# Optimization experiments

Hardware: AMD Instinct MI355X
Metric: run time of the kernel (lower is better)

## Reference

```python
import jax, jax.numpy as jnp
import numpy as np

B, S, D = 4, 2048, 1024
E, F = 8, 4096


def setup_inputs() -> dict:
    key = jax.random.key(0)
    ks = jax.random.split(key, 5)
    x = jax.random.normal(ks[0], (B, S, D), dtype=jnp.float32)
    switch_w = jax.random.normal(ks[1], (D, E), dtype=jnp.float32) * (D ** -0.5)
    switch_b = jnp.zeros((E,), dtype=jnp.float32)
    w1 = jax.random.normal(ks[2], (E, D, F), dtype=jnp.float32) * (D ** -0.5)
    b1 = jnp.zeros((E, F), dtype=jnp.float32)
    w2 = jax.random.normal(ks[3], (E, F, D), dtype=jnp.float32) * (F ** -0.5)
    b2 = jnp.zeros((E, D), dtype=jnp.float32)
    return {"x": x, "switch_w": switch_w, "switch_b": switch_b,
            "w1": w1, "b1": b1, "w2": w2, "b2": b2}


def reference(x, switch_w, switch_b, w1, b1, w2, b2):
    b, s, d = x.shape
    t = x.reshape(-1, d)                                  # [T, D] tokens
    logits = t @ switch_w + switch_b                      # [T, E]
    route_prob = jax.nn.softmax(logits, axis=-1)
    route_prob_max = jnp.max(route_prob, axis=-1)         # [T]
    routes = jnp.argmax(route_prob, axis=-1)              # [T] top-1 expert

    out = jnp.zeros_like(t)
    n_experts = w1.shape[0]
    for e in range(n_experts):                            # small fixed expert loop
        h = jax.nn.gelu(t @ w1[e] + b1[e])                # [T, F]
        y = h @ w2[e] + b2[e]                             # [T, D]
        mask = (routes == e)[:, None]
        out = jnp.where(mask, y, out)                     # scatter-combine by route

    out = out * route_prob_max[:, None]                   # is_scale_prob=True
    return out.reshape(b, s, d)
```

## Files before the change

kernel.cpp:

```cpp
#include <hip/hip_runtime.h>
#include <hip/hip_bf16.h>
#include <math.h>

#define T_TOK 8192
#define DIM   1024
#define NEXP  8
#define FF    4096
#define BM    256
#define BN    256
#define BK    64
#define TPAD  (T_TOK + NEXP * BM)
#define NCBLK 32
#define MT    (TPAD / BM)
#define NG1   640
#define NG2   160
#define NT2   4096

typedef __attribute__((ext_vector_type(4))) float  f32x4;
typedef __attribute__((ext_vector_type(8))) __bf16 bf16x8;
typedef __attribute__((address_space(3))) char ldschar;

__global__ __launch_bounds__(256) void router_kernel(const float* __restrict__ x,
                              const float* __restrict__ sw, const float* __restrict__ sb,
                              int* __restrict__ route, float* __restrict__ scale,
                              __hip_bfloat16* __restrict__ xb)
{
    int wave = threadIdx.x >> 6, lane = threadIdx.x & 63;
    int t = blockIdx.x * 4 + wave;
    const float* xr = x + (size_t)t * DIM + lane * 16;

    float xv[16];
#pragma unroll
    for (int i = 0; i < 4; ++i)
        *(float4*)&xv[i * 4] = *(const float4*)(xr + i * 4);

    bf16x8 u0, u1;
#pragma unroll
    for (int i = 0; i < 8; ++i) { u0[i] = (__bf16)xv[i]; u1[i] = (__bf16)xv[i + 8]; }
    __hip_bfloat16* xo = xb + (size_t)t * DIM + lane * 16;
    *(bf16x8*)xo = u0;
    *(bf16x8*)(xo + 8) = u1;

    double acc[NEXP];
#pragma unroll
    for (int e = 0; e < NEXP; ++e) acc[e] = 0.0;
    const float* swp = sw + lane * 16 * NEXP;
#pragma unroll
    for (int j = 0; j < 16; ++j) {
        float4 s0 = *(const float4*)(swp + j * 8);
        float4 s1 = *(const float4*)(swp + j * 8 + 4);
        double xd = (double)xv[j];
        acc[0] += xd * (double)s0.x; acc[1] += xd * (double)s0.y;
        acc[2] += xd * (double)s0.z; acc[3] += xd * (double)s0.w;
        acc[4] += xd * (double)s1.x; acc[5] += xd * (double)s1.y;
        acc[6] += xd * (double)s1.z; acc[7] += xd * (double)s1.w;
    }
#pragma unroll
    for (int e = 0; e < NEXP; ++e) {
        double v = acc[e];
        for (int off = 32; off; off >>= 1) v += __shfl_down(v, off);
        acc[e] = v;
    }
    if (lane == 0) {
        double m = -1e300; int am = 0;
#pragma unroll
        for (int e = 0; e < NEXP; ++e) {
            double v = acc[e] + (double)sb[e];
            acc[e] = v;
            if (v > m) { m = v; am = e; }
        }
        double s = 0.0;
#pragma unroll
        for (int e = 0; e < NEXP; ++e) s += exp(acc[e] - m);
        route[t] = am;
        scale[t] = (float)(1.0 / s);
    }
}

__global__ __launch_bounds__(256) void count_kernel(const int* __restrict__ route,
                                                    int* __restrict__ bc)
{
    __shared__ int c[NEXP];
    if (threadIdx.x < NEXP) c[threadIdx.x] = 0;
    __syncthreads();
    int t = blockIdx.x * 256 + threadIdx.x;
    atomicAdd(&c[route[t]], 1);
    __syncthreads();
    if (threadIdx.x < NEXP) bc[blockIdx.x * NEXP + threadIdx.x] = c[threadIdx.x];
}

__global__ __launch_bounds__(64) void offsets_kernel(const int* __restrict__ bc,
                                                     int* __restrict__ offPad,
                                                     int* __restrict__ base)
{
    int l = threadIdx.x & 31;
    int cnt[NEXP], pre[NEXP], tot[NEXP];
#pragma unroll
    for (int e = 0; e < NEXP; ++e) cnt[e] = bc[l * NEXP + e];
#pragma unroll
    for (int e = 0; e < NEXP; ++e) {
        int v = cnt[e];
#pragma unroll
        for (int d = 1; d < 32; d <<= 1) {
            int u = __shfl_up(v, d, 32);
            if (l >= d) v += u;
        }
        pre[e] = v - cnt[e];
        tot[e] = __shfl(v, 31, 32);
    }
    int o = 0, off[NEXP];
#pragma unroll
    for (int e = 0; e < NEXP; ++e) {
        off[e] = o;
        o += ((tot[e] + BM - 1) / BM) * BM;
    }
    if (l == 0) {
#pragma unroll
        for (int e = 0; e < NEXP; ++e) offPad[e] = off[e];
        offPad[NEXP] = o;
    }
#pragma unroll
    for (int e = 0; e < NEXP; ++e) base[l * NEXP + e] = off[e] + pre[e];
}

__global__ __launch_bounds__(256) void scatter_kernel(const int* __restrict__ route,
                                                      const int* __restrict__ base,
                                                      int* __restrict__ perm)
{
    __shared__ int cur[NEXP];
    if (threadIdx.x < NEXP) cur[threadIdx.x] = base[blockIdx.x * NEXP + threadIdx.x];
    __syncthreads();
    int t = blockIdx.x * 256 + threadIdx.x;
    int pos = atomicAdd(&cur[route[t]], 1);
    perm[pos] = t;
}

__global__ __launch_bounds__(256) void transpose_cvt64(const float* __restrict__ src,
                                                       __hip_bfloat16* __restrict__ dst,
                                                       int R, int C)
{
    __shared__ float tile[64][65];
    size_t bofs = (size_t)blockIdx.z * (size_t)R * (size_t)C;
    int c0 = blockIdx.x * 64, r0 = blockIdx.y * 64;
    int t = threadIdx.x;
    int tx = t & 15, ty = t >> 4;
#pragma unroll
    for (int i = 0; i < 4; ++i) {
        int r = ty + i * 16;
        float4 v = *(const float4*)(src + bofs + (size_t)(r0 + r) * C + c0 + tx * 4);
        tile[r][tx * 4 + 0] = v.x; tile[r][tx * 4 + 1] = v.y;
        tile[r][tx * 4 + 2] = v.z; tile[r][tx * 4 + 3] = v.w;
    }
    __syncthreads();
    int sx = t & 7, sy = t >> 3;
#pragma unroll
    for (int i = 0; i < 2; ++i) {
        int oc = sy + i * 32;
        bf16x8 u;
#pragma unroll
        for (int j = 0; j < 8; ++j)
            u[j] = (__bf16)tile[sx * 8 + j][oc];
        *(bf16x8*)(dst + bofs + (size_t)(c0 + oc) * R + r0 + sx * 8) = u;
    }
}

#define STAGE_A(b, h, t) do { \
    __builtin_amdgcn_global_load_lds((const __attribute__((address_space(1))) void*)(aSrc[h][0] + (size_t)(t) * 64), \
        (__attribute__((address_space(3))) void*)(ldsA + (b) * 32768 + (h) * 16384 + wid * 1024), 16, 0, 0); \
    __builtin_amdgcn_global_load_lds((const __attribute__((address_space(1))) void*)(aSrc[h][1] + (size_t)(t) * 64), \
        (__attribute__((address_space(3))) void*)(ldsA + (b) * 32768 + (h) * 16384 + (wid + 8) * 1024), 16, 0, 0); \
} while (0)

#define STAGE_B(b, h, t) do { \
    __builtin_amdgcn_global_load_lds((const __attribute__((address_space(1))) void*)(bSrc[h][0] + (size_t)(t) * 64), \
        (__attribute__((address_space(3))) void*)(ldsB + (b) * 32768 + (h) * 16384 + wid * 1024), 16, 0, 0); \
    __builtin_amdgcn_global_load_lds((const __attribute__((address_space(1))) void*)(bSrc[h][1] + (size_t)(t) * 64), \
        (__attribute__((address_space(3))) void*)(ldsB + (b) * 32768 + (h) * 16384 + (wid + 8) * 1024), 16, 0, 0); \
} while (0)

#define VMW asm volatile("s_waitcnt vmcnt(4)" ::: "memory")

#define LDS_FRAG(p) (*(const __attribute__((address_space(3))) bf16x8*)(p))

#define PHASE(B_, MH, KS, LOADB, STAGEX, VMX) do { \
    __builtin_amdgcn_sched_barrier(0); \
    bf16x8 af[4]; \
    _Pragma("unroll") \
    for (int i_ = 0; i_ < 4; ++i_) \
        af[i_] = LDS_FRAG(aRd + (B_) * 32768 + ((MH) * 4 + i_) * 2048 + kOff[KS]); \
    if (LOADB) { \
        _Pragma("unroll") \
        for (int n_ = 0; n_ < 4; ++n_) \
            bfr[KS][n_] = LDS_FRAG(bRd + (B_) * 32768 + n_ * 2048 + kOff[KS]); \
    } \
    STAGEX; \
    __builtin_amdgcn_s_barrier(); \
    asm volatile("s_waitcnt lgkmcnt(0)" ::: "memory"); \
    __builtin_amdgcn_sched_barrier(0); \
    __builtin_amdgcn_s_setprio(1); \
    _Pragma("unroll") \
    for (int i_ = 0; i_ < 4; ++i_) \
        _Pragma("unroll") \
        for (int n_ = 0; n_ < 4; ++n_) \
            acc[(MH) * 4 + i_][n_] = __builtin_amdgcn_mfma_f32_16x16x32_bf16(af[i_], bfr[KS][n_], acc[(MH) * 4 + i_][n_], 0, 0, 0); \
    __builtin_amdgcn_s_setprio(0); \
    VMX; \
    __builtin_amdgcn_s_barrier(); \
} while (0)

template<int MODE>
__global__ __launch_bounds__(512, 2) void moe_gemm8(
    const __hip_bfloat16* __restrict__ A,
    const __hip_bfloat16* __restrict__ Bw,
    const float* __restrict__ bias,
    const int* __restrict__ offPad,
    const int* __restrict__ perm,
    const float* __restrict__ scale,
    __hip_bfloat16* __restrict__ Hout,
    float* __restrict__ Out,
    const float* __restrict__ w2src,
    __hip_bfloat16* __restrict__ w2tdst,
    const int K, const int N)
{
    __shared__ char lds[131072];
    const int tid = threadIdx.x;
    const int bid = blockIdx.x;

    if (MODE == 0 && bid >= NG1) {
        const int j    = bid - NG1;
        const int t2   = tid & 255;
        const int half = tid >> 8;
        const int tile_id = j * 2 + half;
        const int cx = tile_id & 15;
        const int ry = (tile_id >> 4) & 63;
        const int ez = tile_id >> 10;
        float (*tl)[65] = (float (*)[65])(lds + half * 17408);
        const float* src = w2src + (size_t)ez * FF * DIM;
        __hip_bfloat16* dst = w2tdst + (size_t)ez * DIM * FF;
        const int c0 = cx * 64, r0 = ry * 64;
        const int tx = t2 & 15, ty = t2 >> 4;
#pragma unroll
        for (int i = 0; i < 4; ++i) {
            int r = ty + i * 16;
            float4 v = *(const float4*)(src + (size_t)(r0 + r) * DIM + c0 + tx * 4);
            tl[r][tx * 4 + 0] = v.x; tl[r][tx * 4 + 1] = v.y;
            tl[r][tx * 4 + 2] = v.z; tl[r][tx * 4 + 3] = v.w;
        }
        __syncthreads();
        const int sx = t2 & 7, sy = t2 >> 3;
#pragma unroll
        for (int i = 0; i < 2; ++i) {
            int oc = sy + i * 32;
            bf16x8 u;
#pragma unroll
            for (int jj = 0; jj < 8; ++jj)
                u[jj] = (__bf16)tl[sx * 8 + jj][oc];
            *(bf16x8*)(dst + (size_t)(c0 + oc) * FF + r0 + sx * 8) = u;
        }
        return;
    }

    int mt, nt;
    if (MODE == 0) {
        const int swz = (bid & 7) * (NG1 >> 3) + (bid >> 3);
        mt = swz % MT;
        nt = swz / MT;
    } else {
        mt = (bid & 7) + 8 * (bid >> 5);
        nt = (bid >> 3) & 3;
    }
    const int m0 = mt * BM;
    if (m0 >= offPad[NEXP]) return;
    int e = 0;
    while (offPad[e + 1] <= m0) ++e;

    ldschar* ldsA = (ldschar*)lds;
    ldschar* ldsB = (ldschar*)(lds + 65536);

    const int lane = tid & 63;
    const int wid  = tid >> 6;
    const int wr   = wid >> 2;
    const int wc   = wid & 3;
    const int g    = lane >> 4, rl = lane & 15;

    const __hip_bfloat16* Bp = Bw + (size_t)e * (size_t)N * (size_t)K;

    const int l3 = lane >> 3;
    const int colOff = ((lane & 7) ^ l3) * 8;
    const __hip_bfloat16* aSrc[2][2];
    const __hip_bfloat16* bSrc[2][2];
#pragma unroll
    for (int h = 0; h < 2; ++h)
#pragma unroll
        for (int j = 0; j < 2; ++j) {
            int r = (wid + j * 8) * 8 + l3;
            int arow = m0 + h * 128 + r;
            size_t ar;
            if (MODE == 0) { int tk = perm[arow]; ar = (size_t)(tk < 0 ? 0 : tk); }
            else           { ar = (size_t)arow; }
            aSrc[h][j] = A + ar * (size_t)K + colOff;
            bSrc[h][j] = Bp + (size_t)(nt * BN + h * 128 + r) * (size_t)K + colOff;
        }

    const ldschar* aRd = ldsA + wr * 16384 + rl * 128;
    const ldschar* bRd = ldsB + (wc >> 1) * 16384 + (wc & 1) * 8192 + rl * 128;
    int kOff[2];
    kOff[0] = ((0 * 4 + g) ^ (rl & 7)) * 16;
    kOff[1] = ((1 * 4 + g) ^ (rl & 7)) * 16;

    f32x4 acc[8][4];
#pragma unroll
    for (int i = 0; i < 8; ++i)
#pragma unroll
        for (int n = 0; n < 4; ++n) acc[i][n] = (f32x4)0.0f;
    bf16x8 bfr[2][4];

    const int ntiles = K >> 6;

    STAGE_A(0, 0, 0); STAGE_A(0, 1, 0);
    STAGE_B(0, 0, 0); STAGE_B(0, 1, 0);
    STAGE_B(1, 0, 1); STAGE_B(1, 1, 1);
    asm volatile("s_waitcnt vmcnt(4)" ::: "memory");
    __builtin_amdgcn_s_barrier();

    for (int it = 0; it < (ntiles >> 1); ++it) {
        const int t1 = 2 * it + 1;
        const int t2 = 2 * it + 2 < ntiles ? 2 * it + 2 : ntiles - 1;
        const int t3 = 2 * it + 3 < ntiles ? 2 * it + 3 : ntiles - 1;
        PHASE(0, 0, 0, true,  STAGE_A(1, 0, t1), );
        PHASE(0, 0, 1, true,  STAGE_A(1, 1, t1), );
        PHASE(0, 1, 0, false, STAGE_B(0, 0, t2), );
        PHASE(0, 1, 1, false, STAGE_B(0, 1, t2), VMW);
        PHASE(1, 0, 0, true,  STAGE_A(0, 0, t2), );
        PHASE(1, 0, 1, true,  STAGE_A(0, 1, t2), );
        PHASE(1, 1, 0, false, STAGE_B(1, 0, t3), );
        PHASE(1, 1, 1, false, STAGE_B(1, 1, t3), VMW);
    }
    asm volatile("s_waitcnt vmcnt(0)" ::: "memory");

    const int colBase = nt * BN + wc * 64;
    const int rowBase = m0 + wr * 128;
    float bcol[4];
#pragma unroll
    for (int n = 0; n < 4; ++n) bcol[n] = bias[(size_t)e * N + colBase + n * 16 + rl];

    if (MODE == 0) {
#pragma unroll
        for (int m = 0; m < 8; ++m) {
#pragma unroll
            for (int r = 0; r < 4; ++r) {
                int row = rowBase + m * 16 + g * 4 + r;
                __hip_bfloat16* hrow = Hout + (size_t)row * N + colBase;
#pragma unroll
                for (int n = 0; n < 4; ++n) {
                    float v = acc[m][n][r] + bcol[n];
                    float u = -1.5957691216057308f * (v + 0.044715f * v * v * v);
                    float gel = v / (1.f + __expf(u));
                    hrow[n * 16 + rl] = __float2bfloat16(gel);
                }
            }
        }
    } else {
#pragma unroll
        for (int m = 0; m < 8; ++m) {
#pragma unroll
            for (int r = 0; r < 4; ++r) {
                int row = rowBase + m * 16 + g * 4 + r;
                int tk = perm[row];
                if (tk >= 0) {
                    float sc = scale[tk];
                    float* orow = Out + (size_t)tk * N + colBase;
#pragma unroll
                    for (int n = 0; n < 4; ++n)
                        orow[n * 16 + rl] = (acc[m][n][r] + bcol[n]) * sc;
                }
            }
        }
    }
}

extern "C" void kernel_launch(void* const* d_in, const int* in_sizes, int n_in,
                              void* d_out, int out_size, void* d_ws, size_t ws_size,
                              hipStream_t stream)
{
    const float* x  = (const float*)d_in[0];
    const float* sw = (const float*)d_in[1];
    const float* sb = (const float*)d_in[2];
    const float* w1 = (const float*)d_in[3];
    const float* b1 = (const float*)d_in[4];
    const float* w2 = (const float*)d_in[5];
    const float* b2 = (const float*)d_in[6];
    float* out = (float*)d_out;
    char* ws = (char*)d_ws;

    int*   bc     = (int*)(ws + 1024);
    int*   base   = (int*)(ws + 2048);
    int*   offPad = (int*)(ws + 3072);
    int*   route  = (int*)(ws + 4096);
    float* scale  = (float*)(ws + 36864);
    int*   perm   = (int*)(ws + 69632);

    const size_t offXb   = 131072;
    const size_t szXb    = (size_t)T_TOK * DIM * 2;
    const size_t offW1   = offXb + szXb;
    const size_t szW     = (size_t)NEXP * DIM * FF * 2;
    const size_t offW2   = offW1 + szW;
    const size_t szH     = (size_t)TPAD * FF * 2;
    const size_t offHF   = offW2 + szW;
    const size_t needF   = offHF + szH;

    const bool fuseT = ws_size >= needF;

    __hip_bfloat16* xb  = (__hip_bfloat16*)(ws + offXb);
    __hip_bfloat16* w1t = (__hip_bfloat16*)(ws + offW1);
    __hip_bfloat16* w2t = (__hip_bfloat16*)(ws + (fuseT ? offW2 : offW1));
    __hip_bfloat16* h   = (__hip_bfloat16*)(ws + (fuseT ? offHF : offW2));

    hipMemsetAsync(perm, 0xFF, TPAD * 4, stream);

    router_kernel<<<T_TOK / 4, 256, 0, stream>>>(x, sw, sb, route, scale, xb);
    count_kernel<<<NCBLK, 256, 0, stream>>>(route, bc);
    offsets_kernel<<<1, 64, 0, stream>>>(bc, offPad, base);
    scatter_kernel<<<NCBLK, 256, 0, stream>>>(route, base, perm);

    transpose_cvt64<<<dim3(FF / 64, DIM / 64, NEXP), 256, 0, stream>>>(w1, w1t, DIM, FF);

    if (fuseT) {
        moe_gemm8<0><<<NG1 + NT2, 512, 0, stream>>>(
            xb, w1t, b1, offPad, perm, scale, h, nullptr, w2, w2t, DIM, FF);
        moe_gemm8<1><<<NG2, 512, 0, stream>>>(
            h, w2t, b2, offPad, perm, scale, nullptr, out, nullptr, nullptr, FF, DIM);
    } else {
        moe_gemm8<0><<<NG1, 512, 0, stream>>>(
            xb, w1t, b1, offPad, perm, scale, h, nullptr, nullptr, nullptr, DIM, FF);
        transpose_cvt64<<<dim3(DIM / 64, FF / 64, NEXP), 256, 0, stream>>>(w2, w2t, FF, DIM);
        moe_gemm8<1><<<NG2, 512, 0, stream>>>(
            h, w2t, b2, offPad, perm, scale, nullptr, out, nullptr, nullptr, FF, DIM);
    }
}
```

Before: 314.8 us.

## Replace fused GEMM1+W2-transpose grid with persistent per-XCD ticket scheduler

Replaces the oversized grid of GEMM1 tiles plus W2-transpose blocks with a persistent kernel of 256 blocks. Each block pulls work items from a per-XCD atomic ticket counter, taking GEMM1 tiles first and transpose tiles afterwards. The goal is to balance the uneven expert-tile work against transpose work and to avoid block launch overhead and tail imbalance. The cost is an atomic plus a barrier per item, an extra memset, and a fixed item order in which the transposes run after the GEMM tiles.

New measurement: 338.6 us. 1.08x slower.

```diff
diff --git a/kernel.cpp b/kernel.cpp
--- a/kernel.cpp
+++ b/kernel.cpp
@@ -15,6 +15,7 @@
 #define NG1   640
 #define NG2   160
 #define NT2   4096
+#define ITEMS_PER_XCD (80 + 512)
 
 typedef __attribute__((ext_vector_type(4))) float  f32x4;
 typedef __attribute__((ext_vector_type(8))) __bf16 bf16x8;
@@ -208,6 +209,158 @@
     __builtin_amdgcn_s_barrier(); \
 } while (0)
 
+__global__ __launch_bounds__(512, 2) void moe_work1(
+    const __hip_bfloat16* __restrict__ A,
+    const __hip_bfloat16* __restrict__ Bw,
+    const float* __restrict__ bias,
+    const int* __restrict__ offPad,
+    const int* __restrict__ perm,
+    __hip_bfloat16* __restrict__ Hout,
+    const float* __restrict__ w2src,
+    __hip_bfloat16* __restrict__ w2tdst,
+    int* __restrict__ tickets)
+{
+    __shared__ char lds[131072];
+    __shared__ int sItem;
+    const int tid = threadIdx.x;
+    const int xcd = blockIdx.x & 7;
+    int* tk = tickets + xcd;
+
+    const int lane = tid & 63;
+    const int wid  = tid >> 6;
+    const int wr   = wid >> 2;
+    const int wc   = wid & 3;
+    const int g    = lane >> 4, rl = lane & 15;
+    const int l3   = lane >> 3;
+    const int colOff = ((lane & 7) ^ l3) * 8;
+
+    for (;;) {
+        if (tid == 0) sItem = atomicAdd(tk, 1);
+        __syncthreads();
+        const int item = sItem;
+        if (item >= ITEMS_PER_XCD) break;
+
+        if (item >= 80) {
+            const int j    = xcd * 512 + (item - 80);
+            const int t2   = tid & 255;
+            const int half = tid >> 8;
+            const int tile_id = j * 2 + half;
+            const int cx = tile_id & 15;
+            const int ry = (tile_id >> 4) & 63;
+            const int ez = tile_id >> 10;
+            float (*tl)[65] = (float (*)[65])(lds + half * 17408);
+            const float* src = w2src + (size_t)ez * FF * DIM;
+            __hip_bfloat16* dst = w2tdst + (size_t)ez * DIM * FF;
+            const int c0 = cx * 64, r0 = ry * 64;
+            const int tx = t2 & 15, ty = t2 >> 4;
+#pragma unroll
+            for (int i = 0; i < 4; ++i) {
+                int r = ty + i * 16;
+                float4 v = *(const float4*)(src + (size_t)(r0 + r) * DIM + c0 + tx * 4);
+                tl[r][tx * 4 + 0] = v.x; tl[r][tx * 4 + 1] = v.y;
+                tl[r][tx * 4 + 2] = v.z; tl[r][tx * 4 + 3] = v.w;
+            }
+            __syncthreads();
+            const int sx = t2 & 7, sy = t2 >> 3;
+#pragma unroll
+            for (int i = 0; i < 2; ++i) {
+                int oc = sy + i * 32;
+                bf16x8 u;
+#pragma unroll
+                for (int jj = 0; jj < 8; ++jj)
+                    u[jj] = (__bf16)tl[sx * 8 + jj][oc];
+                *(bf16x8*)(dst + (size_t)(c0 + oc) * FF + r0 + sx * 8) = u;
+            }
+            __syncthreads();
+            continue;
+        }
+
+        const int swz = xcd * 80 + item;
+        const int mt = swz % MT;
+        const int nt = swz / MT;
+        const int m0 = mt * BM;
+        if (m0 >= offPad[NEXP]) continue;
+        int e = 0;
+        while (offPad[e + 1] <= m0) ++e;
+
+        ldschar* ldsA = (ldschar*)lds;
+        ldschar* ldsB = (ldschar*)(lds + 65536);
+
+        const __hip_bfloat16* Bp = Bw + (size_t)e * (size_t)FF * (size_t)DIM;
+        const __hip_bfloat16* aSrc[2][2];
+        const __hip_bfloat16* bSrc[2][2];
+#pragma unroll
+        for (int h = 0; h < 2; ++h)
+#pragma unroll
+            for (int j = 0; j < 2; ++j) {
+                int r = (wid + j * 8) * 8 + l3;
+                int arow = m0 + h * 128 + r;
+                int tkn = perm[arow];
+                size_t ar = (size_t)(tkn < 0 ? 0 : tkn);
+                aSrc[h][j] = A + ar * (size_t)DIM + colOff;
+                bSrc[h][j] = Bp + (size_t)(nt * BN + h * 128 + r) * (size_t)DIM + colOff;
+            }
+
+        const ldschar* aRd = ldsA + wr * 16384 + rl * 128;
+        const ldschar* bRd = ldsB + (wc >> 1) * 16384 + (wc & 1) * 8192 + rl * 128;
+        int kOff[2];
+        kOff[0] = ((0 * 4 + g) ^ (rl & 7)) * 16;
+        kOff[1] = ((1 * 4 + g) ^ (rl & 7)) * 16;
+
+        f32x4 acc[8][4];
+#pragma unroll
+        for (int i = 0; i < 8; ++i)
+#pragma unroll
+            for (int n = 0; n < 4; ++n) acc[i][n] = (f32x4)0.0f;
+        bf16x8 bfr[2][4];
+
+        const int ntiles = DIM >> 6;
+
+        STAGE_A(0, 0, 0); STAGE_A(0, 1, 0);
+        STAGE_B(0, 0, 0); STAGE_B(0, 1, 0);
+        STAGE_B(1, 0, 1); STAGE_B(1, 1, 1);
+        asm volatile("s_waitcnt vmcnt(4)" ::: "memory");
+        __builtin_amdgcn_s_barrier();
+
+        for (int it = 0; it < (ntiles >> 1); ++it) {
+            const int t1 = 2 * it + 1;
+            const int t2 = 2 * it + 2 < ntiles ? 2 * it + 2 : ntiles - 1;
+            const int t3 = 2 * it + 3 < ntiles ? 2 * it + 3 : ntiles - 1;
+            PHASE(0, 0, 0, true,  STAGE_A(1, 0, t1), );
+            PHASE(0, 0, 1, true,  STAGE_A(1, 1, t1), );
+            PHASE(0, 1, 0, false, STAGE_B(0, 0, t2), );
+            PHASE(0, 1, 1, false, STAGE_B(0, 1, t2), VMW);
+            PHASE(1, 0, 0, true,  STAGE_A(0, 0, t2), );
+            PHASE(1, 0, 1, true,  STAGE_A(0, 1, t2), );
+            PHASE(1, 1, 0, false, STAGE_B(1, 0, t3), );
+            PHASE(1, 1, 1, false, STAGE_B(1, 1, t3), VMW);
+        }
+        asm volatile("s_waitcnt vmcnt(0)" ::: "memory");
+
+        const int colBase = nt * BN + wc * 64;
+        const int rowBase = m0 + wr * 128;
+        float bcol[4];
+#pragma unroll
+        for (int n = 0; n < 4; ++n) bcol[n] = bias[(size_t)e * FF + colBase + n * 16 + rl];
+
+#pragma unroll
+        for (int m = 0; m < 8; ++m) {
+#pragma unroll
+            for (int r = 0; r < 4; ++r) {
+                int row = rowBase + m * 16 + g * 4 + r;
+                __hip_bfloat16* hrow = Hout + (size_t)row * FF + colBase;
+#pragma unroll
+                for (int n = 0; n < 4; ++n) {
+                    float v = acc[m][n][r] + bcol[n];
+                    float u = -1.5957691216057308f * (v + 0.044715f * v * v * v);
+                    float gel = v / (1.f + __expf(u));
+                    hrow[n * 16 + rl] = __float2bfloat16(gel);
+                }
+            }
+        }
+    }
+}
+
 template<int MODE>
 __global__ __launch_bounds__(512, 2) void moe_gemm8(
     const __hip_bfloat16* __restrict__ A,
@@ -218,47 +371,11 @@
     const float* __restrict__ scale,
     __hip_bfloat16* __restrict__ Hout,
     float* __restrict__ Out,
-    const float* __restrict__ w2src,
-    __hip_bfloat16* __restrict__ w2tdst,
     const int K, const int N)
 {
     __shared__ char lds[131072];
     const int tid = threadIdx.x;
     const int bid = blockIdx.x;
-
-    if (MODE == 0 && bid >= NG1) {
-        const int j    = bid - NG1;
-        const int t2   = tid & 255;
-        const int half = tid >> 8;
-        const int tile_id = j * 2 + half;
-        const int cx = tile_id & 15;
-        const int ry = (tile_id >> 4) & 63;
-        const int ez = tile_id >> 10;
-        float (*tl)[65] = (float (*)[65])(lds + half * 17408);
-        const float* src = w2src + (size_t)ez * FF * DIM;
-        __hip_bfloat16* dst = w2tdst + (size_t)ez * DIM * FF;
-        const int c0 = cx * 64, r0 = ry * 64;
-        const int tx = t2 & 15, ty = t2 >> 4;
-#pragma unroll
-        for (int i = 0; i < 4; ++i) {
-            int r = ty + i * 16;
-            float4 v = *(const float4*)(src + (size_t)(r0 + r) * DIM + c0 + tx * 4);
-            tl[r][tx * 4 + 0] = v.x; tl[r][tx * 4 + 1] = v.y;
-            tl[r][tx * 4 + 2] = v.z; tl[r][tx * 4 + 3] = v.w;
-        }
-        __syncthreads();
-        const int sx = t2 & 7, sy = t2 >> 3;
-#pragma unroll
-        for (int i = 0; i < 2; ++i) {
-            int oc = sy + i * 32;
-            bf16x8 u;
-#pragma unroll
-            for (int jj = 0; jj < 8; ++jj)
-                u[jj] = (__bf16)tl[sx * 8 + jj][oc];
-            *(bf16x8*)(dst + (size_t)(c0 + oc) * FF + r0 + sx * 8) = u;
-        }
-        return;
-    }
 
     int mt, nt;
     if (MODE == 0) {
@@ -393,12 +510,13 @@
     float* out = (float*)d_out;
     char* ws = (char*)d_ws;
 
-    int*   bc     = (int*)(ws + 1024);
-    int*   base   = (int*)(ws + 2048);
-    int*   offPad = (int*)(ws + 3072);
-    int*   route  = (int*)(ws + 4096);
-    float* scale  = (float*)(ws + 36864);
-    int*   perm   = (int*)(ws + 69632);
+    int*   tickets = (int*)(ws + 0);
+    int*   bc      = (int*)(ws + 1024);
+    int*   base    = (int*)(ws + 2048);
+    int*   offPad  = (int*)(ws + 3072);
+    int*   route   = (int*)(ws + 4096);
+    float* scale   = (float*)(ws + 36864);
+    int*   perm    = (int*)(ws + 69632);
 
     const size_t offXb   = 131072;
     const size_t szXb    = (size_t)T_TOK * DIM * 2;
@@ -416,6 +534,7 @@
     __hip_bfloat16* w2t = (__hip_bfloat16*)(ws + (fuseT ? offW2 : offW1));
     __hip_bfloat16* h   = (__hip_bfloat16*)(ws + (fuseT ? offHF : offW2));
 
+    hipMemsetAsync(tickets, 0, 64, stream);
     hipMemsetAsync(perm, 0xFF, TPAD * 4, stream);
 
     router_kernel<<<T_TOK / 4, 256, 0, stream>>>(x, sw, sb, route, scale, xb);
@@ -426,15 +545,15 @@
     transpose_cvt64<<<dim3(FF / 64, DIM / 64, NEXP), 256, 0, stream>>>(w1, w1t, DIM, FF);
 
     if (fuseT) {
-        moe_gemm8<0><<<NG1 + NT2, 512, 0, stream>>>(
-            xb, w1t, b1, offPad, perm, scale, h, nullptr, w2, w2t, DIM, FF);
+        moe_work1<<<256, 512, 0, stream>>>(
+            xb, w1t, b1, offPad, perm, h, w2, w2t, tickets);
         moe_gemm8<1><<<NG2, 512, 0, stream>>>(
-            h, w2t, b2, offPad, perm, scale, nullptr, out, nullptr, nullptr, FF, DIM);
+            h, w2t, b2, offPad, perm, scale, nullptr, out, FF, DIM);
     } else {
         moe_gemm8<0><<<NG1, 512, 0, stream>>>(
-            xb, w1t, b1, offPad, perm, scale, h, nullptr, nullptr, nullptr, DIM, FF);
+            xb, w1t, b1, offPad, perm, scale, h, nullptr, DIM, FF);
         transpose_cvt64<<<dim3(DIM / 64, FF / 64, NEXP), 256, 0, stream>>>(w2, w2t, FF, DIM);
         moe_gemm8<1><<<NG2, 512, 0, stream>>>(
-            h, w2t, b2, offPad, perm, scale, nullptr, out, nullptr, nullptr, FF, DIM);
-    }
-}
+            h, w2t, b2, offPad, perm, scale, nullptr, out, FF, DIM);
+    }
+}
```
